# Performance work log

Measured on AMD Instinct MI355X. Metric: run time of the kernel, lower is better.

## Reference

```python
import jax, jax.numpy as jnp
import numpy as np

NUM_EXPERTS = 8
TOP_K = 2
LB_WEIGHT = 0.01
LN_EPS = 1e-5


def setup_inputs() -> dict:
    key = jax.random.key(0)
    ks = jax.random.split(key, 4)
    B, S, D, H, E = 4, 2048, 1024, 2048, NUM_EXPERTS
    x = jax.random.normal(ks[0], (B, S, D), dtype=jnp.float32)
    gate_w = jax.random.normal(ks[1], (E, D), dtype=jnp.float32) * 0.02
    w1 = jax.random.normal(ks[2], (E, H, D), dtype=jnp.float32) * 0.02
    w2 = jax.random.normal(ks[3], (E, D, H), dtype=jnp.float32) * 0.02
    ln_gamma = jnp.ones((D,), dtype=jnp.float32)
    ln_beta = jnp.zeros((D,), dtype=jnp.float32)
    return {"x": x, "gate_w": gate_w, "w1": w1, "w2": w2,
            "ln_gamma": ln_gamma, "ln_beta": ln_beta}


def reference(x, gate_w, w1, w2, ln_gamma, ln_beta):
    residual = x
    # LayerNorm (eval mode, dropout=0)
    mu = jnp.mean(x, axis=-1, keepdims=True)
    var = jnp.var(x, axis=-1, keepdims=True)
    xn = (x - mu) * jax.lax.rsqrt(var + LN_EPS) * ln_gamma + ln_beta

    # Router: logits [B,S,E], top-k gating with softmax over selected logits
    logits = jnp.einsum('bsd,ed->bse', xn, gate_w)
    top_vals, top_idx = jax.lax.top_k(logits, TOP_K)  # [B,S,K]
    gates = jax.nn.softmax(top_vals, axis=-1)

    # Load-balance aux loss: (std/mean)^2 of mean routing probs (torch std -> ddof=1)
    probs = jax.nn.softmax(logits, axis=-1)
    avg_probs = jnp.mean(probs, axis=(0, 1))  # [E]
    lb_loss = (jnp.std(avg_probs, ddof=1) / (jnp.mean(avg_probs) + 1e-6)) ** 2

    # Expert dispatch/combine: small fixed loop over experts; tokens not
    # routed to expert e get combined gate 0, matching the torch scatter.
    out = jnp.zeros_like(xn)
    for e in range(NUM_EXPERTS):
        ge = jnp.sum(gates * (top_idx == e), axis=-1)  # [B,S]
        h = jax.nn.gelu(jnp.einsum('bsd,hd->bsh', xn, w1[e]), approximate=False)
        y = jnp.einsum('bsh,dh->bsd', h, w2[e])
        out = out + y * ge[..., None]

    return residual + out, lb_loss * LB_WEIGHT
```

## Files before the change

kernel.cpp:

```cpp
#include <hip/hip_runtime.h>

#define T_TOK 8192
#define DIM 1024
#define HID 2048
#define NE 8
#define TK 16384

typedef __bf16 bf16x8 __attribute__((ext_vector_type(8)));
typedef float f32x16 __attribute__((ext_vector_type(16)));

#define OFF_XN      0UL
#define OFF_W1B     16777216UL
#define OFF_W2B     50331648UL
#define OFF_H       83886080UL
#define OFF_ATOK    150994944UL
#define OFF_INV     151060480UL
#define OFF_TOPI    151126016UL
#define OFF_GATES   151158784UL
#define OFF_CPART   151224320UL
#define OFF_PPART   151226368UL
#define OFF_COUNTS  151228416UL
#define OFF_OFFS    151228448UL
#define OFF_CNT2    151228480UL
#define OFF_NT      151228512UL
#define OFF_TMAP    151228544UL

__device__ __forceinline__ unsigned short f2bf(float f) {
    union { float fv; unsigned u; } q; q.fv = f;
    unsigned r = q.u + 0x7fffu + ((q.u >> 16) & 1u);
    return (unsigned short)(r >> 16);
}

__device__ __forceinline__ float bf2f(unsigned short u) {
    union { unsigned u; float f; } q; q.u = ((unsigned)u) << 16;
    return q.f;
}

__device__ __forceinline__ float gelu_fast(float x) {
    float x3 = x * x * x;
    float z2 = 1.5957691216f * (x + 0.044715f * x3);
    float u = __expf(z2);
    float t = 1.0f - 2.0f * __builtin_amdgcn_rcpf(u + 1.0f);
    return 0.5f * x * (1.0f + t);
}

__device__ __forceinline__ int sw8(int r) { return (r ^ (r >> 3)) & 7; }

__device__ __forceinline__ void g2l16(const unsigned short* g, unsigned short* l) {
    __builtin_amdgcn_global_load_lds(
        (const __attribute__((address_space(1))) unsigned int*)g,
        (__attribute__((address_space(3))) unsigned int*)l, 16, 0, 0);
}

__global__ __launch_bounds__(256) void convert_kernel(
    const float4* __restrict__ s1, ushort4* __restrict__ d1, int n1,
    const float4* __restrict__ s2, ushort4* __restrict__ d2, int n2)
{
    int i = blockIdx.x * 256 + threadIdx.x;
    if (i < n1) {
        float4 f = s1[i];
        ushort4 u; u.x = f2bf(f.x); u.y = f2bf(f.y); u.z = f2bf(f.z); u.w = f2bf(f.w);
        d1[i] = u;
    } else {
        int j = i - n1;
        if (j < n2) {
            float4 f = s2[j];
            ushort4 u; u.x = f2bf(f.x); u.y = f2bf(f.y); u.z = f2bf(f.z); u.w = f2bf(f.w);
            d2[j] = u;
        }
    }
}

__global__ __launch_bounds__(256) void ln_router_kernel(
    const float* __restrict__ x, const float* __restrict__ gw,
    const float* __restrict__ gamma, const float* __restrict__ beta,
    unsigned short* __restrict__ xnb, int* __restrict__ top_idx,
    float2* __restrict__ gates, int* __restrict__ counts_partial,
    float* __restrict__ probs_partial)
{
    __shared__ float sprob[8];
    __shared__ int scnt[8];
    int tid = threadIdx.x;
    if (tid < 8) { sprob[tid] = 0.f; scnt[tid] = 0; }
    __syncthreads();

    int wave = tid >> 6, lane = tid & 63;
    int t = blockIdx.x * 4 + wave;
    const float* xt = x + (size_t)t * DIM;

    float v[16];
    float s = 0.f, sq = 0.f;
#pragma unroll
    for (int j = 0; j < 4; j++) {
        float4 f = *(const float4*)(xt + j * 256 + lane * 4);
        v[4*j+0] = f.x; v[4*j+1] = f.y; v[4*j+2] = f.z; v[4*j+3] = f.w;
        s += f.x + f.y + f.z + f.w;
        sq += f.x*f.x + f.y*f.y + f.z*f.z + f.w*f.w;
    }
#pragma unroll
    for (int o = 32; o > 0; o >>= 1) { s += __shfl_xor(s, o); sq += __shfl_xor(sq, o); }
    float mean = s * (1.0f / DIM);
    float var = sq * (1.0f / DIM) - mean * mean;
    float rstd = rsqrtf(var + 1e-5f);

#pragma unroll
    for (int j = 0; j < 4; j++) {
        float4 gm = *(const float4*)(gamma + j * 256 + lane * 4);
        float4 bt = *(const float4*)(beta + j * 256 + lane * 4);
        float x0 = (v[4*j+0] - mean) * rstd * gm.x + bt.x;
        float x1 = (v[4*j+1] - mean) * rstd * gm.y + bt.y;
        float x2 = (v[4*j+2] - mean) * rstd * gm.z + bt.z;
        float x3 = (v[4*j+3] - mean) * rstd * gm.w + bt.w;
        ushort4 u; u.x = f2bf(x0); u.y = f2bf(x1); u.z = f2bf(x2); u.w = f2bf(x3);
        *(ushort4*)(xnb + (size_t)t * DIM + j * 256 + lane * 4) = u;
        v[4*j+0] = x0; v[4*j+1] = x1; v[4*j+2] = x2; v[4*j+3] = x3;
    }

    double part[8];
#pragma unroll
    for (int e = 0; e < 8; e++) {
        double p = 0.0;
        const float* ge = gw + (size_t)e * DIM;
#pragma unroll
        for (int j = 0; j < 4; j++) {
            float4 g = *(const float4*)(ge + j * 256 + lane * 4);
            p += (double)v[4*j+0] * (double)g.x;
            p += (double)v[4*j+1] * (double)g.y;
            p += (double)v[4*j+2] * (double)g.z;
            p += (double)v[4*j+3] * (double)g.w;
        }
        part[e] = p;
    }
#pragma unroll
    for (int o = 32; o > 0; o >>= 1)
#pragma unroll
        for (int e = 0; e < 8; e++) part[e] += __shfl_xor(part[e], o);

    if (lane == 0) {
        double l0 = -1e300; int e0 = -1;
#pragma unroll
        for (int e = 0; e < 8; e++) if (part[e] > l0) { l0 = part[e]; e0 = e; }
        double l1 = -1e300; int e1 = -1;
#pragma unroll
        for (int e = 0; e < 8; e++) if (e != e0 && part[e] > l1) { l1 = part[e]; e1 = e; }
        float d = expf((float)(l1 - l0));
        float g0 = 1.0f / (1.0f + d);
        float g1 = d / (1.0f + d);
        top_idx[t] = e0 | (e1 << 8);
        gates[t] = make_float2(g0, g1);
        atomicAdd(&scnt[e0], 1);
        atomicAdd(&scnt[e1], 1);
        float pe[8]; float sum = 0.f;
#pragma unroll
        for (int e = 0; e < 8; e++) { pe[e] = expf((float)(part[e] - l0)); sum += pe[e]; }
        float inv = 1.0f / sum;
#pragma unroll
        for (int e = 0; e < 8; e++) atomicAdd(&sprob[e], pe[e] * inv);
    }
    __syncthreads();
    if (tid < 8) {
        int bin = (blockIdx.x & 63) * 8 + tid;
        atomicAdd(&probs_partial[bin], sprob[tid]);
        atomicAdd(&counts_partial[bin], scnt[tid]);
    }
}

__global__ void finalize_kernel(const int* __restrict__ counts_partial,
                                const float* __restrict__ probs_partial,
                                int* __restrict__ counts, int* __restrict__ offsets,
                                int* __restrict__ cnt2, int* __restrict__ ntiles,
                                int4* __restrict__ tile_map, float* __restrict__ lb_out)
{
    int tid = threadIdx.x;
    int c[8]; float p[8];
#pragma unroll
    for (int e = 0; e < 8; e++) { c[e] = counts_partial[tid*8+e]; p[e] = probs_partial[tid*8+e]; }
#pragma unroll
    for (int o = 32; o > 0; o >>= 1)
#pragma unroll
        for (int e = 0; e < 8; e++) { c[e] += __shfl_xor(c[e], o); p[e] += __shfl_xor(p[e], o); }

    if (tid == 0) {
        int off = 0, nt = 0;
        for (int e = 0; e < 8; e++) {
            offsets[e] = off; counts[e] = c[e]; cnt2[e] = 0;
            for (int m0 = 0; m0 < c[e]; m0 += 128) tile_map[nt++] = make_int4(e, m0, off, c[e]);
            off += c[e];
        }
        *ntiles = nt;
        float avg[8]; float m = 0.f;
        for (int e = 0; e < 8; e++) { avg[e] = p[e] / (float)T_TOK; m += avg[e]; }
        m *= (1.0f / 8.0f);
        float var = 0.f;
        for (int e = 0; e < 8; e++) { float d = avg[e] - m; var += d * d; }
        var *= (1.0f / 7.0f);
        float mm = m + 1e-6f;
        lb_out[0] = (var / (mm * mm)) * 0.01f;
    }
}

__global__ __launch_bounds__(256) void placement_kernel(
    const int* __restrict__ top_idx,
    const int* __restrict__ offsets, int* __restrict__ cnt2,
    int* __restrict__ atok, int2* __restrict__ inv)
{
    __shared__ int lcnt[8];
    __shared__ int lbase[8];
    __shared__ int ltok[4096];
    int tid = threadIdx.x;
    if (tid < 8) lcnt[tid] = 0;
    __syncthreads();
    int t = blockIdx.x * 256 + tid;
    int pk = top_idx[t];
    int e0 = pk & 255, e1 = (pk >> 8) & 255;
    int p0 = atomicAdd(&lcnt[e0], 1); ltok[e0*512+p0] = t;
    int p1 = atomicAdd(&lcnt[e1], 1); ltok[e1*512+p1] = t;
    __syncthreads();
    if (tid < 8) lbase[tid] = offsets[tid] + atomicAdd(&cnt2[tid], lcnt[tid]);
    __syncthreads();
    for (int e = 0; e < 8; e++) {
        int c = lcnt[e], b = lbase[e];
        for (int i = tid; i < c; i += 256) atok[b+i] = ltok[e*512+i];
    }
    inv[t] = make_int2(lbase[e0] + p0, lbase[e1] + p1);
}

__global__ __launch_bounds__(256) void gemm1_kernel(
    const unsigned short* __restrict__ xnb, const unsigned short* __restrict__ w1b,
    unsigned short* __restrict__ hbuf, const int* __restrict__ atok,
    const int4* __restrict__ tile_map, const int* __restrict__ ntiles)
{
    if ((int)blockIdx.x >= *ntiles) return;
    int4 tm = tile_map[blockIdx.x];
    int e = tm.x, m0 = tm.y, base = tm.z, cnt = tm.w;
    int n0 = blockIdx.y * 128;

    __shared__ unsigned short As[128 * 64];
    __shared__ unsigned short Bs[128 * 64];

    int tid = threadIdx.x, lane = tid & 63, wave = tid >> 6;
    int sg = tid & 7;

    const unsigned short* ap[4];
    const unsigned short* bp[4];
#pragma unroll
    for (int j = 0; j < 4; j++) {
        int r = j * 32 + (tid >> 3);
        int ai = base + m0 + r; if (m0 + r >= cnt) ai = base;
        int tok = atok[ai];
        int ss = (sg ^ sw8(r)) * 8;
        ap[j] = xnb + (size_t)tok * DIM + ss;
        bp[j] = w1b + ((size_t)e * HID + n0 + r) * DIM + ss;
    }

    int wm = (wave >> 1) * 64, wn = (wave & 1) * 64;
    int r32 = lane & 31, hl = lane >> 5;
    int aoff[2][4], boff[2][4];
#pragma unroll
    for (int mi = 0; mi < 2; mi++)
#pragma unroll
        for (int s = 0; s < 4; s++) {
            int m = wm + mi * 32 + r32;
            int seg = s * 2 + hl;
            aoff[mi][s] = m * 64 + ((seg ^ sw8(m)) * 8);
            int n = wn + mi * 32 + r32;
            boff[mi][s] = n * 64 + ((seg ^ sw8(n)) * 8);
        }

    f32x16 acc[2][2] = {};
    for (int k0 = 0; k0 < DIM; k0 += 64) {
        __syncthreads();
#pragma unroll
        for (int j = 0; j < 4; j++) {
            g2l16(ap[j] + k0, &As[(j * 256 + tid) * 8]);
            g2l16(bp[j] + k0, &Bs[(j * 256 + tid) * 8]);
        }
        __syncthreads();
#pragma unroll
        for (int s = 0; s < 4; s++) {
            bf16x8 a0 = *(const bf16x8*)&As[aoff[0][s]];
            bf16x8 a1 = *(const bf16x8*)&As[aoff[1][s]];
            bf16x8 b0 = *(const bf16x8*)&Bs[boff[0][s]];
            bf16x8 b1 = *(const bf16x8*)&Bs[boff[1][s]];
            acc[0][0] = __builtin_amdgcn_mfma_f32_32x32x16_bf16(a0, b0, acc[0][0], 0, 0, 0);
            acc[0][1] = __builtin_amdgcn_mfma_f32_32x32x16_bf16(a0, b1, acc[0][1], 0, 0, 0);
            acc[1][0] = __builtin_amdgcn_mfma_f32_32x32x16_bf16(a1, b0, acc[1][0], 0, 0, 0);
            acc[1][1] = __builtin_amdgcn_mfma_f32_32x32x16_bf16(a1, b1, acc[1][1], 0, 0, 0);
        }
    }

#pragma unroll
    for (int mi = 0; mi < 2; mi++)
#pragma unroll
        for (int ri = 0; ri < 16; ri++) {
            int rowl = (ri & 3) + 8 * (ri >> 2) + 4 * hl;
            int m = wm + mi * 32 + rowl;
            if (m0 + m < cnt) {
                size_t hrow = (size_t)(base + m0 + m) * HID + n0;
#pragma unroll
                for (int ni = 0; ni < 2; ni++)
                    hbuf[hrow + wn + ni * 32 + r32] = f2bf(gelu_fast(acc[mi][ni][ri]));
            }
        }
}

__global__ __launch_bounds__(256) void gemm2_kernel(
    const unsigned short* __restrict__ hbuf, const unsigned short* __restrict__ w2b,
    unsigned short* __restrict__ ybuf,
    const int4* __restrict__ tile_map, const int* __restrict__ ntiles)
{
    if ((int)blockIdx.x >= *ntiles) return;
    int4 tm = tile_map[blockIdx.x];
    int e = tm.x, m0 = tm.y, base = tm.z, cnt = tm.w;
    int n0 = blockIdx.y * 128;

    __shared__ unsigned short As[128 * 64];
    __shared__ unsigned short Bs[128 * 64];

    int tid = threadIdx.x, lane = tid & 63, wave = tid >> 6;
    int sg = tid & 7;

    const unsigned short* ap[4];
    const unsigned short* bp[4];
#pragma unroll
    for (int j = 0; j < 4; j++) {
        int r = j * 32 + (tid >> 3);
        int ai = base + m0 + r; if (m0 + r >= cnt) ai = base;
        int ss = (sg ^ sw8(r)) * 8;
        ap[j] = hbuf + (size_t)ai * HID + ss;
        bp[j] = w2b + ((size_t)e * DIM + n0 + r) * HID + ss;
    }

    int wm = (wave >> 1) * 64, wn = (wave & 1) * 64;
    int r32 = lane & 31, hl = lane >> 5;
    int aoff[2][4], boff[2][4];
#pragma unroll
    for (int mi = 0; mi < 2; mi++)
#pragma unroll
        for (int s = 0; s < 4; s++) {
            int m = wm + mi * 32 + r32;
            int seg = s * 2 + hl;
            aoff[mi][s] = m * 64 + ((seg ^ sw8(m)) * 8);
            int n = wn + mi * 32 + r32;
            boff[mi][s] = n * 64 + ((seg ^ sw8(n)) * 8);
        }

    f32x16 acc[2][2] = {};
    for (int k0 = 0; k0 < HID; k0 += 64) {
        __syncthreads();
#pragma unroll
        for (int j = 0; j < 4; j++) {
            g2l16(ap[j] + k0, &As[(j * 256 + tid) * 8]);
            g2l16(bp[j] + k0, &Bs[(j * 256 + tid) * 8]);
        }
        __syncthreads();
#pragma unroll
        for (int s = 0; s < 4; s++) {
            bf16x8 a0 = *(const bf16x8*)&As[aoff[0][s]];
            bf16x8 a1 = *(const bf16x8*)&As[aoff[1][s]];
            bf16x8 b0 = *(const bf16x8*)&Bs[boff[0][s]];
            bf16x8 b1 = *(const bf16x8*)&Bs[boff[1][s]];
            acc[0][0] = __builtin_amdgcn_mfma_f32_32x32x16_bf16(a0, b0, acc[0][0], 0, 0, 0);
            acc[0][1] = __builtin_amdgcn_mfma_f32_32x32x16_bf16(a0, b1, acc[0][1], 0, 0, 0);
            acc[1][0] = __builtin_amdgcn_mfma_f32_32x32x16_bf16(a1, b0, acc[1][0], 0, 0, 0);
            acc[1][1] = __builtin_amdgcn_mfma_f32_32x32x16_bf16(a1, b1, acc[1][1], 0, 0, 0);
        }
    }

#pragma unroll
    for (int mi = 0; mi < 2; mi++)
#pragma unroll
        for (int ri = 0; ri < 16; ri++) {
            int rowl = (ri & 3) + 8 * (ri >> 2) + 4 * hl;
            int m = wm + mi * 32 + rowl;
            if (m0 + m < cnt) {
                size_t yrow = (size_t)(base + m0 + m) * DIM + n0;
#pragma unroll
                for (int ni = 0; ni < 2; ni++)
                    ybuf[yrow + wn + ni * 32 + r32] = f2bf(acc[mi][ni][ri]);
            }
        }
}

__global__ __launch_bounds__(256) void combine_kernel(
    const float* __restrict__ x, const unsigned short* __restrict__ ybuf,
    const int2* __restrict__ inv, const float2* __restrict__ gates,
    float* __restrict__ out)
{
    int tid = threadIdx.x;
    int wave = tid >> 6, lane = tid & 63;
    int t = blockIdx.x * 4 + wave;
    int2 sl = inv[t];
    float2 g = gates[t];
    const float* xr = x + (size_t)t * DIM;
    const unsigned short* y0 = ybuf + (size_t)sl.x * DIM;
    const unsigned short* y1 = ybuf + (size_t)sl.y * DIM;
    float* orow = out + (size_t)t * DIM;
#pragma unroll
    for (int j = 0; j < 4; j++) {
        int idx = j * 256 + lane * 4;
        float4 xv = *(const float4*)(xr + idx);
        ushort4 a = *(const ushort4*)(y0 + idx);
        ushort4 b = *(const ushort4*)(y1 + idx);
        float4 o;
        o.x = xv.x + g.x * bf2f(a.x) + g.y * bf2f(b.x);
        o.y = xv.y + g.x * bf2f(a.y) + g.y * bf2f(b.y);
        o.z = xv.z + g.x * bf2f(a.z) + g.y * bf2f(b.z);
        o.w = xv.w + g.x * bf2f(a.w) + g.y * bf2f(b.w);
        *(float4*)(orow + idx) = o;
    }
}

extern "C" void kernel_launch(void* const* d_in, const int* in_sizes, int n_in,
                              void* d_out, int out_size, void* d_ws, size_t ws_size,
                              hipStream_t stream) {
    (void)in_sizes; (void)n_in; (void)out_size; (void)ws_size;
    const float* x     = (const float*)d_in[0];
    const float* gw    = (const float*)d_in[1];
    const float* w1    = (const float*)d_in[2];
    const float* w2    = (const float*)d_in[3];
    const float* gamma = (const float*)d_in[4];
    const float* beta  = (const float*)d_in[5];
    float* out = (float*)d_out;
    char* ws = (char*)d_ws;

    unsigned short* xnb  = (unsigned short*)(ws + OFF_XN);
    unsigned short* w1b  = (unsigned short*)(ws + OFF_W1B);
    unsigned short* w2b  = (unsigned short*)(ws + OFF_W2B);
    unsigned short* hbuf = (unsigned short*)(ws + OFF_H);
    unsigned short* ybuf = (unsigned short*)(ws + OFF_W1B);
    int*    atok    = (int*)(ws + OFF_ATOK);
    int2*   inv     = (int2*)(ws + OFF_INV);
    int*    topi    = (int*)(ws + OFF_TOPI);
    float2* gates   = (float2*)(ws + OFF_GATES);
    int*    cpart   = (int*)(ws + OFF_CPART);
    float*  ppart   = (float*)(ws + OFF_PPART);
    int*    counts  = (int*)(ws + OFF_COUNTS);
    int*    offsets = (int*)(ws + OFF_OFFS);
    int*    cnt2    = (int*)(ws + OFF_CNT2);
    int*    ntiles  = (int*)(ws + OFF_NT);
    int4*   tmap    = (int4*)(ws + OFF_TMAP);

    hipMemsetAsync(ws + OFF_CPART, 0, 4096, stream);

    int n1 = (NE * HID * DIM) / 4, n2 = (NE * DIM * HID) / 4;
    convert_kernel<<<(n1 + n2 + 255) / 256, 256, 0, stream>>>(
        (const float4*)w1, (ushort4*)w1b, n1, (const float4*)w2, (ushort4*)w2b, n2);

    ln_router_kernel<<<T_TOK / 4, 256, 0, stream>>>(x, gw, gamma, beta, xnb, topi, gates, cpart, ppart);
    finalize_kernel<<<1, 64, 0, stream>>>(cpart, ppart, counts, offsets, cnt2, ntiles, tmap,
                                          out + (size_t)T_TOK * DIM);
    placement_kernel<<<T_TOK / 256, 256, 0, stream>>>(topi, offsets, cnt2, atok, inv);

    gemm1_kernel<<<dim3(136, HID / 128), 256, 0, stream>>>(xnb, w1b, hbuf, atok, tmap, ntiles);
    gemm2_kernel<<<dim3(136, DIM / 128), 256, 0, stream>>>(hbuf, w2b, ybuf, tmap, ntiles);
    combine_kernel<<<T_TOK / 4, 256, 0, stream>>>(x, ybuf, inv, gates, out);
}
```

Baseline: 434.9 us.

## Pre-shuffle weights into MFMA fragment layout and load GEMM operands directly to registers

The weight conversion kernel now also reorders w1 and w2 into a per-32-row, per-16-k fragment layout matching the MFMA B operand, so each lane can load its bf16x8 slice contiguously. Both expert GEMMs drop shared memory and barriers: each wave loads A rows and pre-shuffled B fragments straight into registers, double-buffered across k-steps. The grid is also swapped so blocks sharing a token tile run adjacently, which may improve L2 reuse of A. This trades LDS reuse across waves for more redundant global/L2 traffic, and raises register pressure.

```diff
diff --git a/kernel.cpp b/kernel.cpp
--- a/kernel.cpp
+++ b/kernel.cpp
@@ -36,6 +36,10 @@
     return q.f;
 }
 
+__device__ __forceinline__ unsigned pack2(float a, float b) {
+    return (unsigned)f2bf(a) | ((unsigned)f2bf(b) << 16);
+}
+
 __device__ __forceinline__ float gelu_fast(float x) {
     float x3 = x * x * x;
     float z2 = 1.5957691216f * (x + 0.044715f * x3);
@@ -44,30 +48,30 @@
     return 0.5f * x * (1.0f + t);
 }
 
-__device__ __forceinline__ int sw8(int r) { return (r ^ (r >> 3)) & 7; }
-
-__device__ __forceinline__ void g2l16(const unsigned short* g, unsigned short* l) {
-    __builtin_amdgcn_global_load_lds(
-        (const __attribute__((address_space(1))) unsigned int*)g,
-        (__attribute__((address_space(3))) unsigned int*)l, 16, 0, 0);
-}
-
-__global__ __launch_bounds__(256) void convert_kernel(
-    const float4* __restrict__ s1, ushort4* __restrict__ d1, int n1,
-    const float4* __restrict__ s2, ushort4* __restrict__ d2, int n2)
-{
-    int i = blockIdx.x * 256 + threadIdx.x;
-    if (i < n1) {
-        float4 f = s1[i];
-        ushort4 u; u.x = f2bf(f.x); u.y = f2bf(f.y); u.z = f2bf(f.z); u.w = f2bf(f.w);
-        d1[i] = u;
-    } else {
-        int j = i - n1;
-        if (j < n2) {
-            float4 f = s2[j];
-            ushort4 u; u.x = f2bf(f.x); u.y = f2bf(f.y); u.z = f2bf(f.z); u.w = f2bf(f.w);
-            d2[j] = u;
-        }
+__global__ __launch_bounds__(256) void shuffle_kernel(
+    const float* __restrict__ src, unsigned short* __restrict__ dst, int N, int K)
+{
+    __shared__ unsigned short ls[32 * 72];
+    int NT = N >> 5, KS = K >> 4;
+    int bid = blockIdx.x;
+    int e = bid / NT, nt = bid % NT;
+    int tid = threadIdx.x;
+    int row = tid >> 3, kq = tid & 7;
+    int ksl = tid >> 6, ln = tid & 63;
+    const float* sp = src + ((size_t)(e * N + nt * 32 + row)) * K + kq * 8;
+    size_t dbase = (((size_t)e * NT + nt) * KS) * 512 + ln * 8;
+
+    for (int kc = 0; kc < K; kc += 64) {
+        float4 f0 = *(const float4*)(sp + kc);
+        float4 f1 = *(const float4*)(sp + kc + 4);
+        uint4 u;
+        u.x = pack2(f0.x, f0.y); u.y = pack2(f0.z, f0.w);
+        u.z = pack2(f1.x, f1.y); u.w = pack2(f1.z, f1.w);
+        *(uint4*)&ls[row * 72 + kq * 8] = u;
+        __syncthreads();
+        uint4 o = *(const uint4*)&ls[(ln & 31) * 72 + ksl * 16 + (ln >> 5) * 8];
+        *(uint4*)&dst[dbase + (size_t)((kc >> 4) + ksl) * 512] = o;
+        __syncthreads();
     }
 }
 
@@ -225,68 +229,61 @@
     inv[t] = make_int2(lbase[e0] + p0, lbase[e1] + p1);
 }
 
+
+#define G_LOAD(buf, k0)                                                              \
+    do {                                                                             \
+        _Pragma("unroll")                                                            \
+        for (int st = 0; st < 4; st++) {                                             \
+            Af[buf][0][st] = *(const bf16x8*)(a0 + (k0) + st * 16);                  \
+            Af[buf][1][st] = *(const bf16x8*)(a1 + (k0) + st * 16);                  \
+            Bf[buf][0][st] = *(const bf16x8*)(b0 + (size_t)(((k0) >> 4) + st) * 512);\
+            Bf[buf][1][st] = *(const bf16x8*)(b1 + (size_t)(((k0) >> 4) + st) * 512);\
+        }                                                                            \
+    } while (0)
+
+#define G_MFMA(buf)                                                                  \
+    do {                                                                             \
+        _Pragma("unroll")                                                            \
+        for (int st = 0; st < 4; st++) {                                             \
+            acc[0][0] = __builtin_amdgcn_mfma_f32_32x32x16_bf16(Af[buf][0][st], Bf[buf][0][st], acc[0][0], 0, 0, 0); \
+            acc[0][1] = __builtin_amdgcn_mfma_f32_32x32x16_bf16(Af[buf][0][st], Bf[buf][1][st], acc[0][1], 0, 0, 0); \
+            acc[1][0] = __builtin_amdgcn_mfma_f32_32x32x16_bf16(Af[buf][1][st], Bf[buf][0][st], acc[1][0], 0, 0, 0); \
+            acc[1][1] = __builtin_amdgcn_mfma_f32_32x32x16_bf16(Af[buf][1][st], Bf[buf][1][st], acc[1][1], 0, 0, 0); \
+        }                                                                            \
+    } while (0)
+
 __global__ __launch_bounds__(256) void gemm1_kernel(
-    const unsigned short* __restrict__ xnb, const unsigned short* __restrict__ w1b,
+    const unsigned short* __restrict__ xnb, const unsigned short* __restrict__ w1s,
     unsigned short* __restrict__ hbuf, const int* __restrict__ atok,
     const int4* __restrict__ tile_map, const int* __restrict__ ntiles)
 {
-    if ((int)blockIdx.x >= *ntiles) return;
-    int4 tm = tile_map[blockIdx.x];
+    if ((int)blockIdx.y >= *ntiles) return;
+    int4 tm = tile_map[blockIdx.y];
     int e = tm.x, m0 = tm.y, base = tm.z, cnt = tm.w;
-    int n0 = blockIdx.y * 128;
-
-    __shared__ unsigned short As[128 * 64];
-    __shared__ unsigned short Bs[128 * 64];
+    int n0 = blockIdx.x * 128;
 
     int tid = threadIdx.x, lane = tid & 63, wave = tid >> 6;
-    int sg = tid & 7;
-
-    const unsigned short* ap[4];
-    const unsigned short* bp[4];
-#pragma unroll
-    for (int j = 0; j < 4; j++) {
-        int r = j * 32 + (tid >> 3);
-        int ai = base + m0 + r; if (m0 + r >= cnt) ai = base;
-        int tok = atok[ai];
-        int ss = (sg ^ sw8(r)) * 8;
-        ap[j] = xnb + (size_t)tok * DIM + ss;
-        bp[j] = w1b + ((size_t)e * HID + n0 + r) * DIM + ss;
-    }
-
     int wm = (wave >> 1) * 64, wn = (wave & 1) * 64;
     int r32 = lane & 31, hl = lane >> 5;
-    int aoff[2][4], boff[2][4];
-#pragma unroll
-    for (int mi = 0; mi < 2; mi++)
-#pragma unroll
-        for (int s = 0; s < 4; s++) {
-            int m = wm + mi * 32 + r32;
-            int seg = s * 2 + hl;
-            aoff[mi][s] = m * 64 + ((seg ^ sw8(m)) * 8);
-            int n = wn + mi * 32 + r32;
-            boff[mi][s] = n * 64 + ((seg ^ sw8(n)) * 8);
-        }
-
+
+    int ra = m0 + wm + r32;      if (ra >= cnt) ra = 0;
+    int rb = m0 + wm + 32 + r32; if (rb >= cnt) rb = 0;
+    int t0 = atok[base + ra], t1 = atok[base + rb];
+    const unsigned short* a0 = xnb + (size_t)t0 * DIM + hl * 8;
+    const unsigned short* a1 = xnb + (size_t)t1 * DIM + hl * 8;
+    int n32 = (n0 + wn) >> 5;
+    const unsigned short* b0 = w1s + (((size_t)e * (HID/32) + n32 + 0) * (DIM/16)) * 512 + lane * 8;
+    const unsigned short* b1 = w1s + (((size_t)e * (HID/32) + n32 + 1) * (DIM/16)) * 512 + lane * 8;
+
+    bf16x8 Af[2][2][4], Bf[2][2][4];
     f32x16 acc[2][2] = {};
-    for (int k0 = 0; k0 < DIM; k0 += 64) {
-        __syncthreads();
-#pragma unroll
-        for (int j = 0; j < 4; j++) {
-            g2l16(ap[j] + k0, &As[(j * 256 + tid) * 8]);
-            g2l16(bp[j] + k0, &Bs[(j * 256 + tid) * 8]);
-        }
-        __syncthreads();
-#pragma unroll
-        for (int s = 0; s < 4; s++) {
-            bf16x8 a0 = *(const bf16x8*)&As[aoff[0][s]];
-            bf16x8 a1 = *(const bf16x8*)&As[aoff[1][s]];
-            bf16x8 b0 = *(const bf16x8*)&Bs[boff[0][s]];
-            bf16x8 b1 = *(const bf16x8*)&Bs[boff[1][s]];
-            acc[0][0] = __builtin_amdgcn_mfma_f32_32x32x16_bf16(a0, b0, acc[0][0], 0, 0, 0);
-            acc[0][1] = __builtin_amdgcn_mfma_f32_32x32x16_bf16(a0, b1, acc[0][1], 0, 0, 0);
-            acc[1][0] = __builtin_amdgcn_mfma_f32_32x32x16_bf16(a1, b0, acc[1][0], 0, 0, 0);
-            acc[1][1] = __builtin_amdgcn_mfma_f32_32x32x16_bf16(a1, b1, acc[1][1], 0, 0, 0);
-        }
+
+    G_LOAD(0, 0);
+    for (int k0 = 0; k0 < DIM; k0 += 128) {
+        G_LOAD(1, k0 + 64);
+        G_MFMA(0);
+        if (k0 + 128 < DIM) G_LOAD(0, k0 + 128);
+        G_MFMA(1);
     }
 
 #pragma unroll
@@ -305,66 +302,36 @@
 }
 
 __global__ __launch_bounds__(256) void gemm2_kernel(
-    const unsigned short* __restrict__ hbuf, const unsigned short* __restrict__ w2b,
+    const unsigned short* __restrict__ hbuf, const unsigned short* __restrict__ w2s,
     unsigned short* __restrict__ ybuf,
     const int4* __restrict__ tile_map, const int* __restrict__ ntiles)
 {
-    if ((int)blockIdx.x >= *ntiles) return;
-    int4 tm = tile_map[blockIdx.x];
+    if ((int)blockIdx.y >= *ntiles) return;
+    int4 tm = tile_map[blockIdx.y];
     int e = tm.x, m0 = tm.y, base = tm.z, cnt = tm.w;
-    int n0 = blockIdx.y * 128;
-
-    __shared__ unsigned short As[128 * 64];
-    __shared__ unsigned short Bs[128 * 64];
+    int n0 = blockIdx.x * 128;
 
     int tid = threadIdx.x, lane = tid & 63, wave = tid >> 6;
-    int sg = tid & 7;
-
-    const unsigned short* ap[4];
-    const unsigned short* bp[4];
-#pragma unroll
-    for (int j = 0; j < 4; j++) {
-        int r = j * 32 + (tid >> 3);
-        int ai = base + m0 + r; if (m0 + r >= cnt) ai = base;
-        int ss = (sg ^ sw8(r)) * 8;
-        ap[j] = hbuf + (size_t)ai * HID + ss;
-        bp[j] = w2b + ((size_t)e * DIM + n0 + r) * HID + ss;
-    }
-
     int wm = (wave >> 1) * 64, wn = (wave & 1) * 64;
     int r32 = lane & 31, hl = lane >> 5;
-    int aoff[2][4], boff[2][4];
-#pragma unroll
-    for (int mi = 0; mi < 2; mi++)
-#pragma unroll
-        for (int s = 0; s < 4; s++) {
-            int m = wm + mi * 32 + r32;
-            int seg = s * 2 + hl;
-            aoff[mi][s] = m * 64 + ((seg ^ sw8(m)) * 8);
-            int n = wn + mi * 32 + r32;
-            boff[mi][s] = n * 64 + ((seg ^ sw8(n)) * 8);
-        }
-
+
+    int ra = m0 + wm + r32;      if (ra >= cnt) ra = 0;
+    int rb = m0 + wm + 32 + r32; if (rb >= cnt) rb = 0;
+    const unsigned short* a0 = hbuf + (size_t)(base + ra) * HID + hl * 8;
+    const unsigned short* a1 = hbuf + (size_t)(base + rb) * HID + hl * 8;
+    int n32 = (n0 + wn) >> 5;
+    const unsigned short* b0 = w2s + (((size_t)e * (DIM/32) + n32 + 0) * (HID/16)) * 512 + lane * 8;
+    const unsigned short* b1 = w2s + (((size_t)e * (DIM/32) + n32 + 1) * (HID/16)) * 512 + lane * 8;
+
+    bf16x8 Af[2][2][4], Bf[2][2][4];
     f32x16 acc[2][2] = {};
-    for (int k0 = 0; k0 < HID; k0 += 64) {
-        __syncthreads();
-#pragma unroll
-        for (int j = 0; j < 4; j++) {
-            g2l16(ap[j] + k0, &As[(j * 256 + tid) * 8]);
-            g2l16(bp[j] + k0, &Bs[(j * 256 + tid) * 8]);
-        }
-        __syncthreads();
-#pragma unroll
-        for (int s = 0; s < 4; s++) {
-            bf16x8 a0 = *(const bf16x8*)&As[aoff[0][s]];
-            bf16x8 a1 = *(const bf16x8*)&As[aoff[1][s]];
-            bf16x8 b0 = *(const bf16x8*)&Bs[boff[0][s]];
-            bf16x8 b1 = *(const bf16x8*)&Bs[boff[1][s]];
-            acc[0][0] = __builtin_amdgcn_mfma_f32_32x32x16_bf16(a0, b0, acc[0][0], 0, 0, 0);
-            acc[0][1] = __builtin_amdgcn_mfma_f32_32x32x16_bf16(a0, b1, acc[0][1], 0, 0, 0);
-            acc[1][0] = __builtin_amdgcn_mfma_f32_32x32x16_bf16(a1, b0, acc[1][0], 0, 0, 0);
-            acc[1][1] = __builtin_amdgcn_mfma_f32_32x32x16_bf16(a1, b1, acc[1][1], 0, 0, 0);
-        }
+
+    G_LOAD(0, 0);
+    for (int k0 = 0; k0 < HID; k0 += 128) {
+        G_LOAD(1, k0 + 64);
+        G_MFMA(0);
+        if (k0 + 128 < HID) G_LOAD(0, k0 + 128);
+        G_MFMA(1);
     }
 
 #pragma unroll
@@ -425,8 +392,8 @@
     char* ws = (char*)d_ws;
 
     unsigned short* xnb  = (unsigned short*)(ws + OFF_XN);
-    unsigned short* w1b  = (unsigned short*)(ws + OFF_W1B);
-    unsigned short* w2b  = (unsigned short*)(ws + OFF_W2B);
+    unsigned short* w1s  = (unsigned short*)(ws + OFF_W1B);
+    unsigned short* w2s  = (unsigned short*)(ws + OFF_W2B);
     unsigned short* hbuf = (unsigned short*)(ws + OFF_H);
     unsigned short* ybuf = (unsigned short*)(ws + OFF_W1B);
     int*    atok    = (int*)(ws + OFF_ATOK);
@@ -443,16 +410,15 @@
 
     hipMemsetAsync(ws + OFF_CPART, 0, 4096, stream);
 
-    int n1 = (NE * HID * DIM) / 4, n2 = (NE * DIM * HID) / 4;
-    convert_kernel<<<(n1 + n2 + 255) / 256, 256, 0, stream>>>(
-        (const float4*)w1, (ushort4*)w1b, n1, (const float4*)w2, (ushort4*)w2b, n2);
+    shuffle_kernel<<<NE * (HID/32), 256, 0, stream>>>(w1, w1s, HID, DIM);
+    shuffle_kernel<<<NE * (DIM/32), 256, 0, stream>>>(w2, w2s, DIM, HID);
 
     ln_router_kernel<<<T_TOK / 4, 256, 0, stream>>>(x, gw, gamma, beta, xnb, topi, gates, cpart, ppart);
     finalize_kernel<<<1, 64, 0, stream>>>(cpart, ppart, counts, offsets, cnt2, ntiles, tmap,
                                           out + (size_t)T_TOK * DIM);
     placement_kernel<<<T_TOK / 256, 256, 0, stream>>>(topi, offsets, cnt2, atok, inv);
 
-    gemm1_kernel<<<dim3(136, HID / 128), 256, 0, stream>>>(xnb, w1b, hbuf, atok, tmap, ntiles);
-    gemm2_kernel<<<dim3(136, DIM / 128), 256, 0, stream>>>(hbuf, w2b, ybuf, tmap, ntiles);
+    gemm1_kernel<<<dim3(HID / 128, 136), 256, 0, stream>>>(xnb, w1s, hbuf, atok, tmap, ntiles);
+    gemm2_kernel<<<dim3(DIM / 128, 136), 256, 0, stream>>>(hbuf, w2s, ybuf, tmap, ntiles);
     combine_kernel<<<T_TOK / 4, 256, 0, stream>>>(x, ybuf, inv, gates, out);
 }
```

Result: slower. 618.8 us (+42.3%).
